# Kernel tuning notes

Measured on AMD Instinct MI355X. Metric: run time of the kernel, lower is better.

## Reference

```python
import jax, jax.numpy as jnp
import numpy as np

LAMBDA1 = 0.3366
LAMBDA2 = 0.2424
LAMBDA3 = 0.06
LR = 0.1
N_ITERS = 10          # fixed iteration count standing in for the eps-based while loop
BETA1, BETA2, ADAM_EPS = 0.9, 0.999, 1e-8


def setup_inputs() -> dict:
    key = jax.random.key(0)
    k1, k2, k3 = jax.random.split(key, 3)
    D, T, K = 512, 50000, 16
    return {
        "embedding": jax.random.normal(k1, (D, T), jnp.float32),
        "basis_init": jax.random.normal(k2, (D, K), jnp.float32),
        "activation_init": jax.random.normal(k3, (K, T), jnp.float32),
        "k": K,
    }


def _matrix_l1(X):
    # torch.linalg.norm(X, ord=1) on a 2D tensor = induced 1-norm = max column abs-sum
    return jnp.max(jnp.sum(jnp.abs(X), axis=0))


def _jitter(A):
    # temporal jitter penalty: sum of abs frame-to-frame differences
    return jnp.sum(jnp.abs(A[:, 1:] - A[:, :-1]))


def _shrink(X):
    # faithful to the (buggy) torch _shrink: sign(X) * max(0, |X - lr*l|)
    return jnp.sign(X) * jnp.maximum(0.0, jnp.abs(X - LR * LAMBDA1))


def _adam(p, g, m, v, t):
    m = BETA1 * m + (1.0 - BETA1) * g
    v = BETA2 * v + (1.0 - BETA2) * g * g
    mh = m / (1.0 - BETA1 ** t)
    vh = v / (1.0 - BETA2 ** t)
    p = p - LR * mh / (jnp.sqrt(vh) + ADAM_EPS)
    return p, m, v


def _run(embedding, basis_init, activation_init):
    A = activation_init  # optimizer_act.step() is never called in the source -> A is constant

    def loss_from_B(B):
        return (_matrix_l1(embedding - B @ A)
                + LAMBDA1 * _matrix_l1(B)
                + LAMBDA2 * _matrix_l1(A)
                + LAMBDA3 * _jitter(A))

    # iteration 1: loss is computed on the raw parameter (shrink applied after the step)
    P = basis_init
    m = jnp.zeros_like(P)
    v = jnp.zeros_like(P)
    g = jax.grad(loss_from_B)(P)
    P, m, v = _adam(P, g, m, v, jnp.float32(1.0))

    # iterations 2..N: loss sees shrink(P); gradient flows through the shrink into P
    def step(carry, t):
        P, m, v = carry
        g = jax.grad(lambda p: loss_from_B(_shrink(p)))(P)
        P, m, v = _adam(P, g, m, v, t)
        return (P, m, v), None

    ts = jnp.arange(2, N_ITERS + 1, dtype=jnp.float32)
    (P, m, v), _ = jax.lax.scan(step, (P, m, v), ts)
    return _shrink(P), A


def reference(embedding, basis_init, activation_init, k):
    # returns (embedding_basis_matrix, activation_matrix) as in OutputDiarization
    return _run(embedding, basis_init, activation_init)
```

## Files before the change

kernel.cpp:

```cpp
#include <hip/hip_runtime.h>

#define D 512
#define T 50000
#define K 16

#define ROWS_PER_SLICE 64
#define N_SLICES (D / ROWS_PER_SLICE)

#define LAMBDA1 0.3366f
#define LR      0.1f
#define SHRINK_C (LR * LAMBDA1)
#define BETA1   0.9f
#define BETA2   0.999f
#define ADAM_EPS 1e-8f

__device__ __forceinline__ float sgn(float x) {
    return (x > 0.f) ? 1.f : ((x < 0.f) ? -1.f : 0.f);
}

__global__ void init_kernel(const float* __restrict__ Pin, float* __restrict__ P,
                            float* __restrict__ m, float* __restrict__ v,
                            float* __restrict__ B, unsigned long long* slot) {
    int idx = blockIdx.x * blockDim.x + threadIdx.x;
    if (idx < D * K) {
        float p = Pin[idx];
        P[idx] = p;
        m[idx] = 0.f;
        v[idx] = 0.f;
        B[idx] = p;
    }
    if (idx == 0) *slot = 0ull;
}

__global__ __launch_bounds__(256) void partial_colsum_kernel(
        const float* __restrict__ E, const float* __restrict__ A,
        const float* __restrict__ B, float* __restrict__ partial) {
    int j = blockIdx.x * blockDim.x + threadIdx.x;
    int s = blockIdx.y;
    if (j >= T) return;

    float a[K];
#pragma unroll
    for (int k = 0; k < K; ++k) a[k] = A[k * T + j];

    int r0 = s * ROWS_PER_SLICE;
    float acc = 0.f;
#pragma unroll 4
    for (int ii = 0; ii < ROWS_PER_SLICE; ++ii) {
        int i = r0 + ii;
        float r = E[i * T + j];
        const float* Br = B + i * K;
#pragma unroll
        for (int k = 0; k < K; ++k) r -= Br[k] * a[k];
        acc += fabsf(r);
    }
    partial[s * T + j] = acc;
}

__global__ __launch_bounds__(256) void reduce_argmax_kernel(
        const float* __restrict__ partial, unsigned long long* slot) {
    int j = blockIdx.x * blockDim.x + threadIdx.x;
    float acc = 0.f;
    if (j < T) {
#pragma unroll
        for (int s = 0; s < N_SLICES; ++s) acc += partial[s * T + j];
    }
    unsigned long long key =
        (((unsigned long long)__float_as_uint(acc)) << 32) | (unsigned int)j;
    if (j >= T) key = 0ull;

#pragma unroll
    for (int off = 32; off > 0; off >>= 1) {
        unsigned long long o = __shfl_down(key, off, 64);
        if (o > key) key = o;
    }
    __shared__ unsigned long long wmax[4];
    int lane = threadIdx.x & 63, wid = threadIdx.x >> 6;
    if (lane == 0) wmax[wid] = key;
    __syncthreads();
    if (threadIdx.x == 0) {
        unsigned long long best = wmax[0];
        for (int w = 1; w < 4; ++w)
            if (wmax[w] > best) best = wmax[w];
        atomicMax(slot, best);
    }
}

__global__ __launch_bounds__(512) void update_kernel(
        const float* __restrict__ E, const float* __restrict__ A,
        float* __restrict__ B, float* __restrict__ P,
        float* __restrict__ m, float* __restrict__ v,
        unsigned long long* slot, float bias1, float bias2, int shrinkGrad) {
    int i = threadIdx.x;
    __shared__ float colB[K];
    __shared__ int js_s, ks_s;
    if (i < K) colB[i] = 0.f;
    if (i == 0) js_s = (int)((*slot) & 0xffffffffull);
    __syncthreads();
    int js = js_s;

    float b[K];
#pragma unroll
    for (int k = 0; k < K; ++k) b[k] = B[i * K + k];

    float r = E[i * T + js];
#pragma unroll
    for (int k = 0; k < K; ++k) r -= b[k] * A[k * T + js];
    float s = sgn(r);

#pragma unroll
    for (int k = 0; k < K; ++k) {
        float x = fabsf(b[k]);
#pragma unroll
        for (int off = 32; off > 0; off >>= 1) x += __shfl_down(x, off, 64);
        if ((threadIdx.x & 63) == 0) atomicAdd(&colB[k], x);
    }
    __syncthreads();
    if (i == 0) {
        int kb = 0;
        float best = colB[0];
        for (int k = 1; k < K; ++k)
            if (colB[k] > best) { best = colB[k]; kb = k; }
        ks_s = kb;
        *slot = 0ull;
    }
    __syncthreads();
    int ks = ks_s;

#pragma unroll
    for (int k = 0; k < K; ++k) {
        float g = -s * A[k * T + js];
        if (k == ks) g += LAMBDA1 * sgn(b[k]);
        float p = P[i * K + k];
        if (shrinkGrad) g *= sgn(p) * sgn(p - SHRINK_C);
        float mm = BETA1 * m[i * K + k] + (1.f - BETA1) * g;
        float vv = BETA2 * v[i * K + k] + (1.f - BETA2) * g * g;
        m[i * K + k] = mm;
        v[i * K + k] = vv;
        p -= LR * (mm / bias1) / (sqrtf(vv / bias2) + ADAM_EPS);
        P[i * K + k] = p;
        B[i * K + k] = sgn(p) * fmaxf(0.f, fabsf(p - SHRINK_C));
    }
}

__global__ void output_kernel(const float* __restrict__ B, const float* __restrict__ A,
                              float4* __restrict__ out) {
    int idx = blockIdx.x * blockDim.x + threadIdx.x;
    const int nB4 = (D * K) / 4;
    const int nTot4 = (D * K + K * T) / 4;
    if (idx < nB4) {
        out[idx] = ((const float4*)B)[idx];
    } else if (idx < nTot4) {
        out[idx] = ((const float4*)A)[idx - nB4];
    }
}

extern "C" void kernel_launch(void* const* d_in, const int* in_sizes, int n_in,
                              void* d_out, int out_size, void* d_ws, size_t ws_size,
                              hipStream_t stream) {
    const float* E   = (const float*)d_in[0];
    const float* Bin = (const float*)d_in[1];
    const float* A   = (const float*)d_in[2];

    float* P = (float*)d_ws;
    float* m = P + D * K;
    float* v = m + D * K;
    float* B = v + D * K;
    unsigned long long* slot = (unsigned long long*)(B + D * K);
    float* partial = (float*)(slot + 2);

    init_kernel<<<(D * K + 255) / 256, 256, 0, stream>>>(Bin, P, m, v, B, slot);

    const int cb = (T + 255) / 256;
    for (int it = 1; it <= 10; ++it) {
        partial_colsum_kernel<<<dim3(cb, N_SLICES), 256, 0, stream>>>(E, A, B, partial);
        reduce_argmax_kernel<<<cb, 256, 0, stream>>>(partial, slot);
        float b1 = 1.f - powf(BETA1, (float)it);
        float b2 = 1.f - powf(BETA2, (float)it);
        update_kernel<<<1, 512, 0, stream>>>(E, A, B, P, m, v, slot, b1, b2,
                                             (it >= 2) ? 1 : 0);
    }

    const int nTot4 = (D * K + K * T) / 4;
    output_kernel<<<(nTot4 + 255) / 256, 256, 0, stream>>>(B, A, (float4*)d_out);
}
```

Baseline: 764.1 us.

## Fuse all iterations into one persistent cooperative kernel with grid syncs

```diff
diff --git a/kernel.cpp b/kernel.cpp
--- a/kernel.cpp
+++ b/kernel.cpp
@@ -1,11 +1,18 @@
 #include <hip/hip_runtime.h>
+#include <hip/hip_cooperative_groups.h>
+
+namespace cg = cooperative_groups;
 
 #define D 512
 #define T 50000
 #define K 16
-
-#define ROWS_PER_SLICE 64
-#define N_SLICES (D / ROWS_PER_SLICE)
+#define NIT 10
+
+#define NBLK 256
+#define BTH  512
+#define COLS_PER_BLOCK 196
+#define NGRP 49
+#define PASSES 2
 
 #define LAMBDA1 0.3366f
 #define LR      0.1f
@@ -18,140 +25,201 @@
     return (x > 0.f) ? 1.f : ((x < 0.f) ? -1.f : 0.f);
 }
 
-__global__ void init_kernel(const float* __restrict__ Pin, float* __restrict__ P,
-                            float* __restrict__ m, float* __restrict__ v,
-                            float* __restrict__ B, unsigned long long* slot) {
-    int idx = blockIdx.x * blockDim.x + threadIdx.x;
-    if (idx < D * K) {
-        float p = Pin[idx];
-        P[idx] = p;
-        m[idx] = 0.f;
-        v[idx] = 0.f;
-        B[idx] = p;
-    }
-    if (idx == 0) *slot = 0ull;
-}
-
-__global__ __launch_bounds__(256) void partial_colsum_kernel(
-        const float* __restrict__ E, const float* __restrict__ A,
-        const float* __restrict__ B, float* __restrict__ partial) {
-    int j = blockIdx.x * blockDim.x + threadIdx.x;
-    int s = blockIdx.y;
-    if (j >= T) return;
-
-    float a[K];
-#pragma unroll
-    for (int k = 0; k < K; ++k) a[k] = A[k * T + j];
-
-    int r0 = s * ROWS_PER_SLICE;
-    float acc = 0.f;
+__global__ __launch_bounds__(BTH, 2) void diar_all(
+        const float* __restrict__ E, const float* __restrict__ Bin,
+        const float* __restrict__ A, float* __restrict__ out,
+        unsigned long long* __restrict__ slot) {
+    __shared__ __align__(16) float Bl[D * K];
+    __shared__ float4 psum[16][32];
+    __shared__ float wsum[8][K];
+    __shared__ float colA[K];
+    __shared__ int js_s, ks_s;
+
+    const int tid = threadIdx.x;
+    const int bid = blockIdx.x;
+    cg::grid_group grid = cg::this_grid();
+
+    float pr[K], mr[K], vr[K];
+    {
+        const float4* src = reinterpret_cast<const float4*>(Bin + tid * K);
+        float4* bl4 = reinterpret_cast<float4*>(&Bl[tid * K]);
+#pragma unroll
+        for (int q = 0; q < 4; ++q) {
+            float4 x = src[q];
+            bl4[q] = x;
+            pr[4 * q + 0] = x.x; pr[4 * q + 1] = x.y;
+            pr[4 * q + 2] = x.z; pr[4 * q + 3] = x.w;
+        }
+#pragma unroll
+        for (int k = 0; k < K; ++k) { mr[k] = 0.f; vr[k] = 0.f; }
+    }
+    if (bid == 0 && tid < NIT) atomicExch(&slot[tid], 0ull);
+    __syncthreads();
+    grid.sync();
+
+    const int c = tid & 31;
+    const int s = tid >> 5;
+
+    float b1p = 1.f, b2p = 1.f;
+
+    for (int it = 1; it <= NIT; ++it) {
+        b1p *= BETA1; b2p *= BETA2;
+
+        unsigned long long key = 0ull;
+#pragma unroll
+        for (int p = 0; p < PASSES; ++p) {
+            const int g = p * 32 + c;
+            const int j0 = bid * COLS_PER_BLOCK + g * 4;
+            const bool ok = (g < NGRP) && (j0 < T);
+            float4 acc = {0.f, 0.f, 0.f, 0.f};
+            if (ok) {
+                float4 a4[K];
+#pragma unroll
+                for (int k = 0; k < K; ++k)
+                    a4[k] = *reinterpret_cast<const float4*>(A + (size_t)k * T + j0);
+                const int rbase = s * 32;
+                const float* Ep = E + j0;
 #pragma unroll 4
-    for (int ii = 0; ii < ROWS_PER_SLICE; ++ii) {
-        int i = r0 + ii;
-        float r = E[i * T + j];
-        const float* Br = B + i * K;
-#pragma unroll
-        for (int k = 0; k < K; ++k) r -= Br[k] * a[k];
-        acc += fabsf(r);
-    }
-    partial[s * T + j] = acc;
-}
-
-__global__ __launch_bounds__(256) void reduce_argmax_kernel(
-        const float* __restrict__ partial, unsigned long long* slot) {
-    int j = blockIdx.x * blockDim.x + threadIdx.x;
-    float acc = 0.f;
-    if (j < T) {
-#pragma unroll
-        for (int s = 0; s < N_SLICES; ++s) acc += partial[s * T + j];
-    }
-    unsigned long long key =
-        (((unsigned long long)__float_as_uint(acc)) << 32) | (unsigned int)j;
-    if (j >= T) key = 0ull;
-
-#pragma unroll
-    for (int off = 32; off > 0; off >>= 1) {
-        unsigned long long o = __shfl_down(key, off, 64);
-        if (o > key) key = o;
-    }
-    __shared__ unsigned long long wmax[4];
-    int lane = threadIdx.x & 63, wid = threadIdx.x >> 6;
-    if (lane == 0) wmax[wid] = key;
-    __syncthreads();
-    if (threadIdx.x == 0) {
-        unsigned long long best = wmax[0];
-        for (int w = 1; w < 4; ++w)
-            if (wmax[w] > best) best = wmax[w];
-        atomicMax(slot, best);
-    }
-}
-
-__global__ __launch_bounds__(512) void update_kernel(
-        const float* __restrict__ E, const float* __restrict__ A,
-        float* __restrict__ B, float* __restrict__ P,
-        float* __restrict__ m, float* __restrict__ v,
-        unsigned long long* slot, float bias1, float bias2, int shrinkGrad) {
-    int i = threadIdx.x;
-    __shared__ float colB[K];
-    __shared__ int js_s, ks_s;
-    if (i < K) colB[i] = 0.f;
-    if (i == 0) js_s = (int)((*slot) & 0xffffffffull);
-    __syncthreads();
-    int js = js_s;
-
-    float b[K];
-#pragma unroll
-    for (int k = 0; k < K; ++k) b[k] = B[i * K + k];
-
-    float r = E[i * T + js];
-#pragma unroll
-    for (int k = 0; k < K; ++k) r -= b[k] * A[k * T + js];
-    float s = sgn(r);
-
-#pragma unroll
-    for (int k = 0; k < K; ++k) {
-        float x = fabsf(b[k]);
-#pragma unroll
-        for (int off = 32; off > 0; off >>= 1) x += __shfl_down(x, off, 64);
-        if ((threadIdx.x & 63) == 0) atomicAdd(&colB[k], x);
-    }
-    __syncthreads();
-    if (i == 0) {
-        int kb = 0;
-        float best = colB[0];
-        for (int k = 1; k < K; ++k)
-            if (colB[k] > best) { best = colB[k]; kb = k; }
-        ks_s = kb;
-        *slot = 0ull;
-    }
-    __syncthreads();
-    int ks = ks_s;
-
-#pragma unroll
-    for (int k = 0; k < K; ++k) {
-        float g = -s * A[k * T + js];
-        if (k == ks) g += LAMBDA1 * sgn(b[k]);
-        float p = P[i * K + k];
-        if (shrinkGrad) g *= sgn(p) * sgn(p - SHRINK_C);
-        float mm = BETA1 * m[i * K + k] + (1.f - BETA1) * g;
-        float vv = BETA2 * v[i * K + k] + (1.f - BETA2) * g * g;
-        m[i * K + k] = mm;
-        v[i * K + k] = vv;
-        p -= LR * (mm / bias1) / (sqrtf(vv / bias2) + ADAM_EPS);
-        P[i * K + k] = p;
-        B[i * K + k] = sgn(p) * fmaxf(0.f, fabsf(p - SHRINK_C));
-    }
-}
-
-__global__ void output_kernel(const float* __restrict__ B, const float* __restrict__ A,
-                              float4* __restrict__ out) {
-    int idx = blockIdx.x * blockDim.x + threadIdx.x;
-    const int nB4 = (D * K) / 4;
-    const int nTot4 = (D * K + K * T) / 4;
-    if (idx < nB4) {
-        out[idx] = ((const float4*)B)[idx];
-    } else if (idx < nTot4) {
-        out[idx] = ((const float4*)A)[idx - nB4];
+                for (int ii = 0; ii < 32; ++ii) {
+                    const int i = rbase + ii;
+                    const float4 e = *reinterpret_cast<const float4*>(Ep + (size_t)i * T);
+                    const float4* br = reinterpret_cast<const float4*>(&Bl[i * K]);
+                    float bb[K];
+                    *reinterpret_cast<float4*>(&bb[0])  = br[0];
+                    *reinterpret_cast<float4*>(&bb[4])  = br[1];
+                    *reinterpret_cast<float4*>(&bb[8])  = br[2];
+                    *reinterpret_cast<float4*>(&bb[12]) = br[3];
+                    float4 r = e;
+#pragma unroll
+                    for (int k = 0; k < K; ++k) {
+                        r.x = fmaf(-bb[k], a4[k].x, r.x);
+                        r.y = fmaf(-bb[k], a4[k].y, r.y);
+                        r.z = fmaf(-bb[k], a4[k].z, r.z);
+                        r.w = fmaf(-bb[k], a4[k].w, r.w);
+                    }
+                    acc.x += fabsf(r.x); acc.y += fabsf(r.y);
+                    acc.z += fabsf(r.z); acc.w += fabsf(r.w);
+                }
+            }
+            psum[s][c] = acc;
+            __syncthreads();
+            if (tid < 32) {
+                const int gg = p * 32 + tid;
+                const int jb = bid * COLS_PER_BLOCK + gg * 4;
+                if (gg < NGRP && jb < T) {
+                    float4 cs = psum[0][tid];
+#pragma unroll
+                    for (int q = 1; q < 16; ++q) {
+                        float4 pq = psum[q][tid];
+                        cs.x += pq.x; cs.y += pq.y; cs.z += pq.z; cs.w += pq.w;
+                    }
+                    float v4[4] = {cs.x, cs.y, cs.z, cs.w};
+#pragma unroll
+                    for (int q = 0; q < 4; ++q) {
+                        unsigned long long kq =
+                            (((unsigned long long)__float_as_uint(v4[q])) << 32)
+                            | (unsigned int)(jb + q);
+                        if (kq > key) key = kq;
+                    }
+                }
+            }
+            __syncthreads();
+        }
+        if (tid < 64) {
+#pragma unroll
+            for (int off = 32; off > 0; off >>= 1) {
+                unsigned long long o = __shfl_down(key, off, 64);
+                if (o > key) key = o;
+            }
+            if (tid == 0) atomicMax(&slot[it - 1], key);
+        }
+
+        grid.sync();
+
+        if (tid == 0) {
+            unsigned long long kk = atomicMax(&slot[it - 1], 0ull);
+            js_s = (int)(kk & 0xffffffffull);
+        }
+        __syncthreads();
+        const int js = js_s;
+        if (tid < K) colA[tid] = A[(size_t)tid * T + js];
+
+        float cb[K];
+        {
+            const float* brow = &Bl[tid * K];
+#pragma unroll
+            for (int k = 0; k < K; ++k) cb[k] = fabsf(brow[k]);
+#pragma unroll
+            for (int off = 32; off > 0; off >>= 1) {
+#pragma unroll
+                for (int k = 0; k < K; ++k) cb[k] += __shfl_down(cb[k], off, 64);
+            }
+            if ((tid & 63) == 0) {
+                const int w = tid >> 6;
+#pragma unroll
+                for (int k = 0; k < K; ++k) wsum[w][k] = cb[k];
+            }
+        }
+        __syncthreads();
+        if (tid == 0) {
+            float best = -1.f; int kb = 0;
+#pragma unroll
+            for (int k = 0; k < K; ++k) {
+                float t = 0.f;
+                for (int w = 0; w < 8; ++w) t += wsum[w][k];
+                if (t > best) { best = t; kb = k; }
+            }
+            ks_s = kb;
+        }
+        __syncthreads();
+        const int ks = ks_s;
+        const float biasm = 1.f - b1p;
+        const float biasv = 1.f - b2p;
+
+        float r = E[(size_t)tid * T + js];
+        const float* brow = &Bl[tid * K];
+#pragma unroll
+        for (int k = 0; k < K; ++k) r = fmaf(-brow[k], colA[k], r);
+        const float sg = sgn(r);
+
+#pragma unroll
+        for (int k = 0; k < K; ++k) {
+            float g = -sg * colA[k];
+            if (k == ks) g += LAMBDA1 * sgn(brow[k]);
+            float p = pr[k];
+            if (it >= 2) g *= sgn(p) * sgn(p - SHRINK_C);
+            float mm = BETA1 * mr[k] + (1.f - BETA1) * g;
+            float vv = BETA2 * vr[k] + (1.f - BETA2) * g * g;
+            mr[k] = mm; vr[k] = vv;
+            p -= LR * (mm / biasm) / (sqrtf(vv / biasv) + ADAM_EPS);
+            pr[k] = p;
+        }
+        {
+            float4* bl4 = reinterpret_cast<float4*>(&Bl[tid * K]);
+#pragma unroll
+            for (int q = 0; q < 4; ++q) {
+                float4 x;
+                x.x = sgn(pr[4 * q + 0]) * fmaxf(0.f, fabsf(pr[4 * q + 0] - SHRINK_C));
+                x.y = sgn(pr[4 * q + 1]) * fmaxf(0.f, fabsf(pr[4 * q + 1] - SHRINK_C));
+                x.z = sgn(pr[4 * q + 2]) * fmaxf(0.f, fabsf(pr[4 * q + 2] - SHRINK_C));
+                x.w = sgn(pr[4 * q + 3]) * fmaxf(0.f, fabsf(pr[4 * q + 3] - SHRINK_C));
+                bl4[q] = x;
+            }
+        }
+        __syncthreads();
+    }
+
+    if (bid == 0) {
+        float4* o4 = reinterpret_cast<float4*>(out);
+        const float4* b4 = reinterpret_cast<const float4*>(Bl);
+#pragma unroll
+        for (int q = 0; q < 4; ++q) o4[tid * 4 + q] = b4[tid * 4 + q];
+    }
+    {
+        float4* o4 = reinterpret_cast<float4*>(out) + (D * K) / 4;
+        const float4* a4p = reinterpret_cast<const float4*>(A);
+        const int n4 = (K * T) / 4;
+        for (int q = bid * BTH + tid; q < n4; q += NBLK * BTH) o4[q] = a4p[q];
     }
 }
 
@@ -161,26 +229,10 @@
     const float* E   = (const float*)d_in[0];
     const float* Bin = (const float*)d_in[1];
     const float* A   = (const float*)d_in[2];
-
-    float* P = (float*)d_ws;
-    float* m = P + D * K;
-    float* v = m + D * K;
-    float* B = v + D * K;
-    unsigned long long* slot = (unsigned long long*)(B + D * K);
-    float* partial = (float*)(slot + 2);
-
-    init_kernel<<<(D * K + 255) / 256, 256, 0, stream>>>(Bin, P, m, v, B, slot);
-
-    const int cb = (T + 255) / 256;
-    for (int it = 1; it <= 10; ++it) {
-        partial_colsum_kernel<<<dim3(cb, N_SLICES), 256, 0, stream>>>(E, A, B, partial);
-        reduce_argmax_kernel<<<cb, 256, 0, stream>>>(partial, slot);
-        float b1 = 1.f - powf(BETA1, (float)it);
-        float b2 = 1.f - powf(BETA2, (float)it);
-        update_kernel<<<1, 512, 0, stream>>>(E, A, B, P, m, v, slot, b1, b2,
-                                             (it >= 2) ? 1 : 0);
-    }
-
-    const int nTot4 = (D * K + K * T) / 4;
-    output_kernel<<<(nTot4 + 255) / 256, 256, 0, stream>>>(B, A, (float4*)d_out);
+    float* out = (float*)d_out;
+    unsigned long long* slot = (unsigned long long*)d_ws;
+
+    void* args[] = { (void*)&E, (void*)&Bin, (void*)&A, (void*)&out, (void*)&slot };
+    hipLaunchCooperativeKernel((void*)diar_all, dim3(NBLK), dim3(BTH),
+                               args, 0, stream);
 }
```

After: 860.0 us. 12.6% more time.
